# Performance work log

Measured on AMD Instinct MI355X. Metric: run time of the kernel, lower is better.

Reference implementation:

```python
import jax, jax.numpy as jnp
import numpy as np

N_EMBD = 1024
N_HEADS = 16
HEAD_DIM = N_EMBD // N_HEADS


def setup_inputs() -> dict:
    key = jax.random.key(0)
    ks = jax.random.split(key, 12)
    B, T, S, C = 2, 2048, 2048, N_EMBD
    std = 1.0 / np.sqrt(C)
    inp = {
        "x": jax.random.normal(ks[0], (B, T, C), dtype=jnp.float32),
        "context": jax.random.normal(ks[1], (B, S, C), dtype=jnp.float32),
        "q_w": jax.random.uniform(ks[2], (C, C), minval=-std, maxval=std, dtype=jnp.float32),
        "q_b": jax.random.uniform(ks[3], (C,), minval=-std, maxval=std, dtype=jnp.float32),
        "k_w": jax.random.uniform(ks[4], (C, C), minval=-std, maxval=std, dtype=jnp.float32),
        "k_b": jax.random.uniform(ks[5], (C,), minval=-std, maxval=std, dtype=jnp.float32),
        "v_w": jax.random.uniform(ks[6], (C, C), minval=-std, maxval=std, dtype=jnp.float32),
        "v_b": jax.random.uniform(ks[7], (C,), minval=-std, maxval=std, dtype=jnp.float32),
        "o_w": jax.random.uniform(ks[8], (C, C), minval=-std, maxval=std, dtype=jnp.float32),
        "o_b": jax.random.uniform(ks[9], (C,), minval=-std, maxval=std, dtype=jnp.float32),
    }
    return inp


def reference(x, context, q_w, q_b, k_w, k_b, v_w, v_b, o_w, o_b):
    B, T, C = x.shape
    S = context.shape[1]
    H, D = N_HEADS, HEAD_DIM
    # projections (torch Linear: y = x @ W^T + b; here weights stored as [in, out])
    q = (x @ q_w + q_b).reshape(B, T, H, D).transpose(0, 2, 1, 3)        # [B,H,T,D]
    k = (context @ k_w + k_b).reshape(B, S, H, D).transpose(0, 2, 1, 3)  # [B,H,S,D]
    v = (context @ v_w + v_b).reshape(B, S, H, D).transpose(0, 2, 1, 3)  # [B,H,S,D]
    att = jnp.einsum("bhtd,bhsd->bhts", q, k) / jnp.sqrt(jnp.float32(D))  # [B,H,T,S]
    causal = jnp.tril(jnp.ones((T, S), dtype=bool))                       # mask from tril buffer
    att = jnp.where(causal[None, None, :, :], att, -jnp.inf)
    att = jax.nn.softmax(att, axis=-1)
    y = jnp.einsum("bhts,bhsd->bhtd", att, v)                             # [B,H,T,D]
    y = y.transpose(0, 2, 1, 3).reshape(B, T, C)
    return y @ o_w + o_b
```

## Files before the change

### kernel.cpp

```cpp
#include <hip/hip_runtime.h>
#include <hip/hip_bf16.h>

using bf16 = __bf16;
using bf16x4 = __attribute__((ext_vector_type(4))) __bf16;
using bf16x8 = __attribute__((ext_vector_type(8))) __bf16;
using f32x4 = __attribute__((ext_vector_type(4))) float;

#define EXP2F(x) __builtin_amdgcn_exp2f(x)

__global__ __launch_bounds__(256) void cvt_kernel(const float4* __restrict__ a,
                                                  const float4* __restrict__ b,
                                                  bf16x4* __restrict__ out) {
  int g = blockIdx.x * blockDim.x + threadIdx.x;
  float4 v = (g < 1048576) ? a[g] : b[g - 1048576];
  bf16x4 o = {(bf16)v.x, (bf16)v.y, (bf16)v.z, (bf16)v.w};
  out[g] = o;
}

__global__ __launch_bounds__(256) void transpose_kernel(const float* __restrict__ w0,
                                                        const float* __restrict__ w1,
                                                        const float* __restrict__ w2,
                                                        const float* __restrict__ w3,
                                                        bf16* __restrict__ wtbase) {
  __shared__ float tile[32][33];
  const int z = blockIdx.z;
  const float* w = (z == 0) ? w0 : (z == 1) ? w1 : (z == 2) ? w2 : w3;
  bf16* wt = wtbase + (size_t)z * 1048576;
  int k0 = blockIdx.y * 32, n0 = blockIdx.x * 32;
  int tx = threadIdx.x, ty = threadIdx.y;
#pragma unroll
  for (int i = 0; i < 4; i++)
    tile[ty + i * 8][tx] = w[(size_t)(k0 + ty + i * 8) * 1024 + n0 + tx];
  __syncthreads();
#pragma unroll
  for (int i = 0; i < 4; i++)
    wt[(size_t)(n0 + ty + i * 8) * 1024 + k0 + tx] = (bf16)tile[tx][ty + i * 8];
}

__device__ __forceinline__ void gemm_body(const bf16* __restrict__ A,
                                          const bf16* __restrict__ Bt,
                                          const float* __restrict__ bias,
                                          void* __restrict__ outp, int mode, int bx, int by) {
  constexpr int K = 1024;
  __shared__ __align__(16) char smem[34816];
  bf16(*As)[40] = (bf16(*)[40])smem;
  bf16(*Bs)[40] = (bf16(*)[40])(smem + 10240);
  bf16(*Cs)[136] = (bf16(*)[136])smem;

  const int tid = threadIdx.x;
  const int lane = tid & 63;
  const int w = tid >> 6;
  const int wr = w >> 1, wc = w & 1;
  const int m0 = by * 128, n0 = bx * 128;
  const int fr = lane & 15, fg = (lane >> 4) * 8;

  f32x4 acc[4][4] = {};

  const int srow = tid >> 2;
  const int kc = (tid & 3) * 8;
  const int arow = m0 + srow, brow = n0 + srow;

  bf16x8 ra0, ra1, rb0, rb1;
  ra0 = *(const bf16x8*)&A[(size_t)arow * K + kc];
  ra1 = *(const bf16x8*)&A[(size_t)(arow + 64) * K + kc];
  rb0 = *(const bf16x8*)&Bt[(size_t)brow * K + kc];
  rb1 = *(const bf16x8*)&Bt[(size_t)(brow + 64) * K + kc];

  for (int k0 = 0; k0 < K; k0 += 32) {
    __syncthreads();
    *(bf16x8*)&As[srow][kc] = ra0;
    *(bf16x8*)&As[srow + 64][kc] = ra1;
    *(bf16x8*)&Bs[srow][kc] = rb0;
    *(bf16x8*)&Bs[srow + 64][kc] = rb1;
    if (k0 + 32 < K) {
      int kn = k0 + 32 + kc;
      ra0 = *(const bf16x8*)&A[(size_t)arow * K + kn];
      ra1 = *(const bf16x8*)&A[(size_t)(arow + 64) * K + kn];
      rb0 = *(const bf16x8*)&Bt[(size_t)brow * K + kn];
      rb1 = *(const bf16x8*)&Bt[(size_t)(brow + 64) * K + kn];
    }
    __syncthreads();
    bf16x8 af[4], bfr[4];
#pragma unroll
    for (int mi = 0; mi < 4; mi++)
      af[mi] = *(const bf16x8*)&As[wr * 64 + mi * 16 + fr][fg];
#pragma unroll
    for (int ni = 0; ni < 4; ni++)
      bfr[ni] = *(const bf16x8*)&Bs[wc * 64 + ni * 16 + fr][fg];
#pragma unroll
    for (int mi = 0; mi < 4; mi++)
#pragma unroll
      for (int ni = 0; ni < 4; ni++)
        acc[mi][ni] =
            __builtin_amdgcn_mfma_f32_16x16x32_bf16(af[mi], bfr[ni], acc[mi][ni], 0, 0, 0);
  }

  float bv[4];
#pragma unroll
  for (int ni = 0; ni < 4; ni++) bv[ni] = bias[n0 + wc * 64 + ni * 16 + fr];
#pragma unroll
  for (int mi = 0; mi < 4; mi++)
#pragma unroll
    for (int ni = 0; ni < 4; ni++)
#pragma unroll
      for (int j = 0; j < 4; j++) acc[mi][ni][j] += bv[ni];

  if (mode == 2) {
    float* O = (float*)outp;
#pragma unroll
    for (int mi = 0; mi < 4; mi++)
#pragma unroll
      for (int ni = 0; ni < 4; ni++)
#pragma unroll
        for (int j = 0; j < 4; j++) {
          int row = m0 + wr * 64 + mi * 16 + (lane >> 4) * 4 + j;
          int col = n0 + wc * 64 + ni * 16 + fr;
          O[(size_t)row * 1024 + col] = acc[mi][ni][j];
        }
    return;
  }

  __syncthreads();
#pragma unroll
  for (int mi = 0; mi < 4; mi++) {
    int r = wr * 64 + mi * 16 + (lane >> 4) * 4;
#pragma unroll
    for (int ni = 0; ni < 4; ni++) {
      int c = wc * 64 + ni * 16 + fr;
#pragma unroll
      for (int j = 0; j < 4; j++) Cs[r + j][c] = (bf16)acc[mi][ni][j];
    }
  }
  __syncthreads();

  bf16* O = (bf16*)outp;
  if (mode == 0) {
    int row = tid >> 1, ch = (tid & 1) * 64;
    int rg = m0 + row;
    int b = rg >> 11, t_ = rg & 2047;
    int c0 = n0 + ch;
    int h = c0 >> 6;
    bf16* dst = O + ((size_t)(b * 16 + h) * 2048 + t_) * 64;
#pragma unroll
    for (int i = 0; i < 8; i++) *(bf16x8*)&dst[i * 8] = *(const bf16x8*)&Cs[row][ch + i * 8];
  } else {
    int colL = tid >> 1, sh = (tid & 1) * 64;
    int cg = n0 + colL;
    int h = cg >> 6, d = cg & 63;
    int rg = m0 + sh;
    int b = rg >> 11, s_ = rg & 2047;
    bf16* dst = O + ((size_t)((b * 16 + h) * 64 + d)) * 2048 + s_;
#pragma unroll
    for (int i = 0; i < 8; i++) {
      bf16x8 v;
#pragma unroll
      for (int jj = 0; jj < 8; jj++) v[jj] = Cs[sh + i * 8 + jj][colL];
      *(bf16x8*)&dst[i * 8] = v;
    }
  }
}

__global__ __launch_bounds__(256) void gemm_qkv_kernel(const bf16* __restrict__ xb,
                                                       const bf16* __restrict__ cb,
                                                       const bf16* __restrict__ wtbase,
                                                       const float* __restrict__ bq,
                                                       const float* __restrict__ bk,
                                                       const float* __restrict__ bv,
                                                       bf16* __restrict__ outbase) {
  const int z = blockIdx.z;
  const bf16* A = (z == 0) ? xb : cb;
  const bf16* Wt = wtbase + (size_t)z * 1048576;
  const float* bias = (z == 0) ? bq : (z == 1) ? bk : bv;
  bf16* out = outbase + (size_t)z * 4194304;
  gemm_body(A, Wt, bias, (void*)out, (z == 2) ? 1 : 0, blockIdx.x, blockIdx.y);
}

__global__ __launch_bounds__(256) void gemm_o_kernel(const bf16* __restrict__ A,
                                                     const bf16* __restrict__ Wt,
                                                     const float* __restrict__ bias,
                                                     float* __restrict__ out) {
  gemm_body(A, Wt, bias, (void*)out, 2, blockIdx.x, blockIdx.y);
}

__global__ __launch_bounds__(256) void attn_kernel(const bf16* __restrict__ Q,
                                                   const bf16* __restrict__ Kc,
                                                   const bf16* __restrict__ Vt,
                                                   bf16* __restrict__ Y) {
  const int bh = blockIdx.x;
  const int qt = 31 - blockIdx.y;
  const int tid = threadIdx.x, lane = tid & 63, w = tid >> 6;
  const int lr = lane & 15, lg = lane >> 4;
  const int q0 = qt * 64 + w * 16;

  __shared__ __align__(16) bf16 Ks[64 * 64];
  __shared__ __align__(16) bf16 Vs[64 * 64];
  __shared__ __align__(16) bf16 Plds[4][16][72];

  const bf16* qb = Q + ((size_t)bh * 2048 + q0 + lr) * 64 + lg * 8;
  const bf16x8 qfB0 = *(const bf16x8*)qb;
  const bf16x8 qfB1 = *(const bf16x8*)(qb + 32);

  const bf16* Kbase = Kc + (size_t)bh * 2048 * 64;
  const bf16* Vbase = Vt + (size_t)bh * 64 * 2048;

  const int srow = tid >> 2;
  const int scol = (tid & 3) * 16;
  const int r7x = (srow & 7) * 8;
  const int d0 = srow * 64 + (scol ^ r7x);
  const int d1 = srow * 64 + ((scol + 8) ^ r7x);

  bf16x8 kr0, kr1, vr0, vr1;
  {
    const bf16* kp = Kbase + (size_t)srow * 64 + scol;
    kr0 = *(const bf16x8*)kp;
    kr1 = *(const bf16x8*)(kp + 8);
    const bf16* vp = Vbase + (size_t)srow * 2048 + scol;
    vr0 = *(const bf16x8*)vp;
    vr1 = *(const bf16x8*)(vp + 8);
  }

  f32x4 yacc[4] = {};
  float mrow = -__builtin_inff(), lrow = 0.0f;
  const float SCL = 0.125f * 1.4426950408889634f;
  const int kxor = (lr & 7) * 8;

  for (int c = 0; c <= qt; ++c) {
    const int sbase = c * 64;
    __syncthreads();
    *(bf16x8*)&Ks[d0] = kr0;
    *(bf16x8*)&Ks[d1] = kr1;
    *(bf16x8*)&Vs[d0] = vr0;
    *(bf16x8*)&Vs[d1] = vr1;
    __syncthreads();

    {
      const int cn = (c < qt) ? c + 1 : c;
      const int sb = cn * 64;
      const bf16* kp = Kbase + (size_t)(sb + srow) * 64 + scol;
      kr0 = *(const bf16x8*)kp;
      kr1 = *(const bf16x8*)(kp + 8);
      const bf16* vp = Vbase + (size_t)srow * 2048 + sb + scol;
      vr0 = *(const bf16x8*)vp;
      vr1 = *(const bf16x8*)(vp + 8);
    }

    f32x4 st[4];
#pragma unroll
    for (int h = 0; h < 4; ++h) {
      const int rb = (16 * h + lr) * 64;
      const bf16x8 kf0 = *(const bf16x8*)&Ks[rb + ((lg * 8) ^ kxor)];
      const bf16x8 kf1 = *(const bf16x8*)&Ks[rb + ((32 + lg * 8) ^ kxor)];
      f32x4 z = {};
      z = __builtin_amdgcn_mfma_f32_16x16x32_bf16(kf0, qfB0, z, 0, 0, 0);
      z = __builtin_amdgcn_mfma_f32_16x16x32_bf16(kf1, qfB1, z, 0, 0, 0);
      st[h] = z;
    }
#pragma unroll
    for (int h = 0; h < 4; ++h)
#pragma unroll
      for (int j = 0; j < 4; ++j) st[h][j] *= SCL;
    if (c == qt) {
      const int qg = q0 + lr;
#pragma unroll
      for (int h = 0; h < 4; ++h)
#pragma unroll
        for (int j = 0; j < 4; ++j) {
          int sg = sbase + 16 * h + lg * 4 + j;
          if (sg > qg) st[h][j] = -__builtin_inff();
        }
    }
    float vmax = fmaxf(fmaxf(st[0][0], st[0][1]), fmaxf(st[0][2], st[0][3]));
#pragma unroll
    for (int h = 1; h < 4; ++h)
      vmax = fmaxf(vmax, fmaxf(fmaxf(st[h][0], st[h][1]), fmaxf(st[h][2], st[h][3])));
    vmax = fmaxf(vmax, __shfl_xor(vmax, 16));
    vmax = fmaxf(vmax, __shfl_xor(vmax, 32));

    if (!__all(vmax <= mrow)) {
      const float mnew = fmaxf(mrow, vmax);
      const float cf = EXP2F(mrow - mnew);
      mrow = mnew;
      lrow *= cf;
      float cfj[4];
#pragma unroll
      for (int j = 0; j < 4; ++j) cfj[j] = __shfl(cf, lg * 4 + j);
#pragma unroll
      for (int nf = 0; nf < 4; ++nf)
#pragma unroll
        for (int j = 0; j < 4; ++j) yacc[nf][j] *= cfj[j];
    }

    float rs = 0.0f;
#pragma unroll
    for (int h = 0; h < 4; ++h) {
      float p0 = EXP2F(st[h][0] - mrow);
      float p1 = EXP2F(st[h][1] - mrow);
      float p2 = EXP2F(st[h][2] - mrow);
      float p3 = EXP2F(st[h][3] - mrow);
      rs += (p0 + p1) + (p2 + p3);
      bf16x4 pk = {(bf16)p0, (bf16)p1, (bf16)p2, (bf16)p3};
      *(bf16x4*)&Plds[w][lr][16 * h + lg * 4] = pk;
    }
    rs += __shfl_xor(rs, 16);
    rs += __shfl_xor(rs, 32);
    lrow += rs;

    const bf16x8 pa0 = *(const bf16x8*)&Plds[w][lr][lg * 8];
    const bf16x8 pa1 = *(const bf16x8*)&Plds[w][lr][32 + lg * 8];
#pragma unroll
    for (int nf = 0; nf < 4; ++nf) {
      const int rb = (nf * 16 + lr) * 64;
      const bf16x8 vf0 = *(const bf16x8*)&Vs[rb + ((lg * 8) ^ kxor)];
      const bf16x8 vf1 = *(const bf16x8*)&Vs[rb + ((32 + lg * 8) ^ kxor)];
      yacc[nf] = __builtin_amdgcn_mfma_f32_16x16x32_bf16(pa0, vf0, yacc[nf], 0, 0, 0);
      yacc[nf] = __builtin_amdgcn_mfma_f32_16x16x32_bf16(pa1, vf1, yacc[nf], 0, 0, 0);
    }
  }

  const float rinv = 1.0f / lrow;
  float linv[4];
#pragma unroll
  for (int j = 0; j < 4; ++j) linv[j] = __shfl(rinv, lg * 4 + j);
  const int b = bh >> 4, h = bh & 15;
#pragma unroll
  for (int nf = 0; nf < 4; ++nf)
#pragma unroll
    for (int j = 0; j < 4; ++j) {
      int qg = q0 + lg * 4 + j;
      Y[((size_t)b * 2048 + qg) * 1024 + h * 64 + nf * 16 + lr] = (bf16)(yacc[nf][j] * linv[j]);
    }
}

extern "C" void kernel_launch(void* const* d_in, const int* in_sizes, int n_in,
                              void* d_out, int out_size, void* d_ws, size_t ws_size,
                              hipStream_t stream) {
  const float* x = (const float*)d_in[0];
  const float* ctx = (const float*)d_in[1];
  const float* q_w = (const float*)d_in[2];
  const float* q_b = (const float*)d_in[3];
  const float* k_w = (const float*)d_in[4];
  const float* k_b = (const float*)d_in[5];
  const float* v_w = (const float*)d_in[6];
  const float* v_b = (const float*)d_in[7];
  const float* o_w = (const float*)d_in[8];
  const float* o_b = (const float*)d_in[9];

  char* ws = (char*)d_ws;
  const size_t MB = 1024 * 1024;
  bf16* xb = (bf16*)(ws + 0);
  bf16* qwt = (bf16*)(ws + 16 * MB);
  bf16* Qws = (bf16*)(ws + 24 * MB);
  bf16* Kws = (bf16*)(ws + 32 * MB);
  bf16* Vt = (bf16*)(ws + 40 * MB);
  bf16* Yws = (bf16*)(ws + 48 * MB);
  bf16* owt = qwt + 3 * 1048576;

  cvt_kernel<<<8192, 256, 0, stream>>>((const float4*)x, (const float4*)ctx, (bf16x4*)xb);

  dim3 tb(32, 8), tg(32, 32, 4);
  transpose_kernel<<<tg, tb, 0, stream>>>(q_w, k_w, v_w, o_w, qwt);

  bf16* cb = xb + (size_t)4096 * 1024 / 2 * 2;
  cb = xb + 4194304;
  gemm_qkv_kernel<<<dim3(8, 32, 3), 256, 0, stream>>>(xb, cb, qwt, q_b, k_b, v_b, Qws);

  attn_kernel<<<dim3(32, 32), 256, 0, stream>>>(Qws, Kws, Vt, Yws);

  gemm_o_kernel<<<dim3(8, 32), 256, 0, stream>>>(Yws, owt, o_b, (float*)d_out);
}
```

Baseline: 127.1 us.

## Remap GEMM blocks per XCD and split attention into 32-row query tiles

The QKV and output GEMMs now launch on a 1D grid and remap each block index so that consecutive tiles land on the same XCD, which should improve L2 locality on the multi-die GPU. The attention kernel moves from 64-row query tiles with 4 waves to 32-row tiles with 2 waves (128 threads). This doubles the block count and gives finer causal load balance. The trade-off is that each K/V chunk loaded into shared memory is now reused by half as many query rows, so total K/V load traffic goes up.

```diff
diff --git a/kernel.cpp b/kernel.cpp
--- a/kernel.cpp
+++ b/kernel.cpp
@@ -167,34 +167,44 @@
                                                        const float* __restrict__ bk,
                                                        const float* __restrict__ bv,
                                                        bf16* __restrict__ outbase) {
-  const int z = blockIdx.z;
+  const int lin = blockIdx.x;
+  const int xcd = lin & 7, idx = lin >> 3;
+  const int seq = xcd * 96 + idx;
+  const int z = seq >> 8;
+  const int rem = seq & 255;
+  const int by = rem >> 3, bx = rem & 7;
   const bf16* A = (z == 0) ? xb : cb;
   const bf16* Wt = wtbase + (size_t)z * 1048576;
   const float* bias = (z == 0) ? bq : (z == 1) ? bk : bv;
   bf16* out = outbase + (size_t)z * 4194304;
-  gemm_body(A, Wt, bias, (void*)out, (z == 2) ? 1 : 0, blockIdx.x, blockIdx.y);
+  gemm_body(A, Wt, bias, (void*)out, (z == 2) ? 1 : 0, bx, by);
 }
 
 __global__ __launch_bounds__(256) void gemm_o_kernel(const bf16* __restrict__ A,
                                                      const bf16* __restrict__ Wt,
                                                      const float* __restrict__ bias,
                                                      float* __restrict__ out) {
-  gemm_body(A, Wt, bias, (void*)out, 2, blockIdx.x, blockIdx.y);
-}
-
-__global__ __launch_bounds__(256) void attn_kernel(const bf16* __restrict__ Q,
+  const int lin = blockIdx.x;
+  const int xcd = lin & 7, idx = lin >> 3;
+  const int seq = xcd * 32 + idx;
+  const int by = seq >> 3, bx = seq & 7;
+  gemm_body(A, Wt, bias, (void*)out, 2, bx, by);
+}
+
+__global__ __launch_bounds__(128) void attn_kernel(const bf16* __restrict__ Q,
                                                    const bf16* __restrict__ Kc,
                                                    const bf16* __restrict__ Vt,
                                                    bf16* __restrict__ Y) {
   const int bh = blockIdx.x;
-  const int qt = 31 - blockIdx.y;
+  const int tile = 63 - blockIdx.y;
+  const int q0t = tile * 32;
   const int tid = threadIdx.x, lane = tid & 63, w = tid >> 6;
   const int lr = lane & 15, lg = lane >> 4;
-  const int q0 = qt * 64 + w * 16;
+  const int q0 = q0t + w * 16;
 
   __shared__ __align__(16) bf16 Ks[64 * 64];
   __shared__ __align__(16) bf16 Vs[64 * 64];
-  __shared__ __align__(16) bf16 Plds[4][16][72];
+  __shared__ __align__(16) bf16 Plds[2][16][72];
 
   const bf16* qb = Q + ((size_t)bh * 2048 + q0 + lr) * 64 + lg * 8;
   const bf16x8 qfB0 = *(const bf16x8*)qb;
@@ -203,45 +213,50 @@
   const bf16* Kbase = Kc + (size_t)bh * 2048 * 64;
   const bf16* Vbase = Vt + (size_t)bh * 64 * 2048;
 
-  const int srow = tid >> 2;
-  const int scol = (tid & 3) * 16;
+  const int srow = tid >> 1;
+  const int scol = (tid & 1) * 32;
   const int r7x = (srow & 7) * 8;
-  const int d0 = srow * 64 + (scol ^ r7x);
-  const int d1 = srow * 64 + ((scol + 8) ^ r7x);
-
-  bf16x8 kr0, kr1, vr0, vr1;
+  int dk[4];
+#pragma unroll
+  for (int i = 0; i < 4; ++i) dk[i] = srow * 64 + ((scol + i * 8) ^ r7x);
+
+  bf16x8 kr[4], vr[4];
   {
     const bf16* kp = Kbase + (size_t)srow * 64 + scol;
-    kr0 = *(const bf16x8*)kp;
-    kr1 = *(const bf16x8*)(kp + 8);
     const bf16* vp = Vbase + (size_t)srow * 2048 + scol;
-    vr0 = *(const bf16x8*)vp;
-    vr1 = *(const bf16x8*)(vp + 8);
+#pragma unroll
+    for (int i = 0; i < 4; ++i) {
+      kr[i] = *(const bf16x8*)(kp + i * 8);
+      vr[i] = *(const bf16x8*)(vp + i * 8);
+    }
   }
 
   f32x4 yacc[4] = {};
   float mrow = -__builtin_inff(), lrow = 0.0f;
   const float SCL = 0.125f * 1.4426950408889634f;
   const int kxor = (lr & 7) * 8;
-
-  for (int c = 0; c <= qt; ++c) {
+  const int nchunk = (q0t >> 6) + 1;
+
+  for (int c = 0; c < nchunk; ++c) {
     const int sbase = c * 64;
     __syncthreads();
-    *(bf16x8*)&Ks[d0] = kr0;
-    *(bf16x8*)&Ks[d1] = kr1;
-    *(bf16x8*)&Vs[d0] = vr0;
-    *(bf16x8*)&Vs[d1] = vr1;
+#pragma unroll
+    for (int i = 0; i < 4; ++i) {
+      *(bf16x8*)&Ks[dk[i]] = kr[i];
+      *(bf16x8*)&Vs[dk[i]] = vr[i];
+    }
     __syncthreads();
 
     {
-      const int cn = (c < qt) ? c + 1 : c;
+      const int cn = (c + 1 < nchunk) ? c + 1 : c;
       const int sb = cn * 64;
       const bf16* kp = Kbase + (size_t)(sb + srow) * 64 + scol;
-      kr0 = *(const bf16x8*)kp;
-      kr1 = *(const bf16x8*)(kp + 8);
       const bf16* vp = Vbase + (size_t)srow * 2048 + sb + scol;
-      vr0 = *(const bf16x8*)vp;
-      vr1 = *(const bf16x8*)(vp + 8);
+#pragma unroll
+      for (int i = 0; i < 4; ++i) {
+        kr[i] = *(const bf16x8*)(kp + i * 8);
+        vr[i] = *(const bf16x8*)(vp + i * 8);
+      }
     }
 
     f32x4 st[4];
@@ -259,7 +274,7 @@
     for (int h = 0; h < 4; ++h)
 #pragma unroll
       for (int j = 0; j < 4; ++j) st[h][j] *= SCL;
-    if (c == qt) {
+    if (c == nchunk - 1) {
       const int qg = q0 + lr;
 #pragma unroll
       for (int h = 0; h < 4; ++h)
@@ -354,17 +369,16 @@
   bf16* Vt = (bf16*)(ws + 40 * MB);
   bf16* Yws = (bf16*)(ws + 48 * MB);
   bf16* owt = qwt + 3 * 1048576;
+  bf16* cb = xb + 4194304;
 
   cvt_kernel<<<8192, 256, 0, stream>>>((const float4*)x, (const float4*)ctx, (bf16x4*)xb);
 
   dim3 tb(32, 8), tg(32, 32, 4);
   transpose_kernel<<<tg, tb, 0, stream>>>(q_w, k_w, v_w, o_w, qwt);
 
-  bf16* cb = xb + (size_t)4096 * 1024 / 2 * 2;
-  cb = xb + 4194304;
-  gemm_qkv_kernel<<<dim3(8, 32, 3), 256, 0, stream>>>(xb, cb, qwt, q_b, k_b, v_b, Qws);
-
-  attn_kernel<<<dim3(32, 32), 256, 0, stream>>>(Qws, Kws, Vt, Yws);
-
-  gemm_o_kernel<<<dim3(8, 32), 256, 0, stream>>>(Yws, owt, o_b, (float*)d_out);
-}
+  gemm_qkv_kernel<<<768, 256, 0, stream>>>(xb, cb, qwt, q_b, k_b, v_b, Qws);
+
+  attn_kernel<<<dim3(32, 64), 128, 0, stream>>>(Qws, Kws, Vt, Yws);
+
+  gemm_o_kernel<<<256, 256, 0, stream>>>(Yws, owt, o_b, (float*)d_out);
+}
```

Result: slower. 130.7 us (+2.8%).

## Fuse fp32-to-bf16 activation conversion into QKV GEMM, remap blocks per XCD

Applied to the files above, without the earlier changes.

Removes the separate cvt kernel: the QKV GEMM now loads fp32 activations directly and converts them to bf16 in registers. This avoids writing and re-reading a bf16 copy of x and context, though each GEMM tile now re-reads fp32 data at twice the byte width. The softmax scale is also folded into the Q projection epilogue, removing a multiply per score in the attention loop. Both GEMMs switch to a 1D grid whose block index is remapped so that consecutive tiles land on the same XCD, which is meant to improve L2 reuse.

```diff
diff --git a/kernel.cpp b/kernel.cpp
--- a/kernel.cpp
+++ b/kernel.cpp
@@ -7,15 +7,6 @@
 using f32x4 = __attribute__((ext_vector_type(4))) float;
 
 #define EXP2F(x) __builtin_amdgcn_exp2f(x)
-
-__global__ __launch_bounds__(256) void cvt_kernel(const float4* __restrict__ a,
-                                                  const float4* __restrict__ b,
-                                                  bf16x4* __restrict__ out) {
-  int g = blockIdx.x * blockDim.x + threadIdx.x;
-  float4 v = (g < 1048576) ? a[g] : b[g - 1048576];
-  bf16x4 o = {(bf16)v.x, (bf16)v.y, (bf16)v.z, (bf16)v.w};
-  out[g] = o;
-}
 
 __global__ __launch_bounds__(256) void transpose_kernel(const float* __restrict__ w0,
                                                         const float* __restrict__ w1,
@@ -37,10 +28,12 @@
     wt[(size_t)(n0 + ty + i * 8) * 1024 + k0 + tx] = (bf16)tile[tx][ty + i * 8];
 }
 
-__device__ __forceinline__ void gemm_body(const bf16* __restrict__ A,
+template <int MODE, bool AF32>
+__device__ __forceinline__ void gemm_body(const void* __restrict__ Ap,
                                           const bf16* __restrict__ Bt,
                                           const float* __restrict__ bias,
-                                          void* __restrict__ outp, int mode, int bx, int by) {
+                                          void* __restrict__ outp, int bx, int by,
+                                          float oscale) {
   constexpr int K = 1024;
   __shared__ __align__(16) char smem[34816];
   bf16(*As)[40] = (bf16(*)[40])smem;
@@ -60,9 +53,23 @@
   const int kc = (tid & 3) * 8;
   const int arow = m0 + srow, brow = n0 + srow;
 
+  auto loadA = [&](int row, int kcol) -> bf16x8 {
+    if constexpr (AF32) {
+      const float* Af = (const float*)Ap;
+      float4 u = *(const float4*)&Af[(size_t)row * K + kcol];
+      float4 v = *(const float4*)&Af[(size_t)row * K + kcol + 4];
+      bf16x8 r = {(bf16)u.x, (bf16)u.y, (bf16)u.z, (bf16)u.w,
+                  (bf16)v.x, (bf16)v.y, (bf16)v.z, (bf16)v.w};
+      return r;
+    } else {
+      const bf16* Ab = (const bf16*)Ap;
+      return *(const bf16x8*)&Ab[(size_t)row * K + kcol];
+    }
+  };
+
   bf16x8 ra0, ra1, rb0, rb1;
-  ra0 = *(const bf16x8*)&A[(size_t)arow * K + kc];
-  ra1 = *(const bf16x8*)&A[(size_t)(arow + 64) * K + kc];
+  ra0 = loadA(arow, kc);
+  ra1 = loadA(arow + 64, kc);
   rb0 = *(const bf16x8*)&Bt[(size_t)brow * K + kc];
   rb1 = *(const bf16x8*)&Bt[(size_t)(brow + 64) * K + kc];
 
@@ -74,8 +81,8 @@
     *(bf16x8*)&Bs[srow + 64][kc] = rb1;
     if (k0 + 32 < K) {
       int kn = k0 + 32 + kc;
-      ra0 = *(const bf16x8*)&A[(size_t)arow * K + kn];
-      ra1 = *(const bf16x8*)&A[(size_t)(arow + 64) * K + kn];
+      ra0 = loadA(arow, kn);
+      ra1 = loadA(arow + 64, kn);
       rb0 = *(const bf16x8*)&Bt[(size_t)brow * K + kn];
       rb1 = *(const bf16x8*)&Bt[(size_t)(brow + 64) * K + kn];
     }
@@ -103,9 +110,9 @@
 #pragma unroll
     for (int ni = 0; ni < 4; ni++)
 #pragma unroll
-      for (int j = 0; j < 4; j++) acc[mi][ni][j] += bv[ni];
-
-  if (mode == 2) {
+      for (int j = 0; j < 4; j++) acc[mi][ni][j] = (acc[mi][ni][j] + bv[ni]) * oscale;
+
+  if (MODE == 2) {
     float* O = (float*)outp;
 #pragma unroll
     for (int mi = 0; mi < 4; mi++)
@@ -134,7 +141,7 @@
   __syncthreads();
 
   bf16* O = (bf16*)outp;
-  if (mode == 0) {
+  if (MODE == 0) {
     int row = tid >> 1, ch = (tid & 1) * 64;
     int rg = m0 + row;
     int b = rg >> 11, t_ = rg & 2047;
@@ -160,26 +167,39 @@
   }
 }
 
-__global__ __launch_bounds__(256) void gemm_qkv_kernel(const bf16* __restrict__ xb,
-                                                       const bf16* __restrict__ cb,
+__global__ __launch_bounds__(256) void gemm_qkv_kernel(const float* __restrict__ x,
+                                                       const float* __restrict__ ctx,
                                                        const bf16* __restrict__ wtbase,
                                                        const float* __restrict__ bq,
                                                        const float* __restrict__ bk,
                                                        const float* __restrict__ bv,
                                                        bf16* __restrict__ outbase) {
-  const int z = blockIdx.z;
-  const bf16* A = (z == 0) ? xb : cb;
+  const int lin = blockIdx.x;
+  const int xcd = lin & 7, idx = lin >> 3;
+  const int seq = xcd * 96 + idx;
+  const int z = seq >> 8;
+  const int rem = seq & 255;
+  const int by = rem >> 3, bx = rem & 7;
+  const float* A = (z == 0) ? x : ctx;
   const bf16* Wt = wtbase + (size_t)z * 1048576;
   const float* bias = (z == 0) ? bq : (z == 1) ? bk : bv;
   bf16* out = outbase + (size_t)z * 4194304;
-  gemm_body(A, Wt, bias, (void*)out, (z == 2) ? 1 : 0, blockIdx.x, blockIdx.y);
+  const float oscale = (z == 0) ? 0.125f * 1.4426950408889634f : 1.0f;
+  if (z == 2)
+    gemm_body<1, true>(A, Wt, bias, (void*)out, bx, by, oscale);
+  else
+    gemm_body<0, true>(A, Wt, bias, (void*)out, bx, by, oscale);
 }
 
 __global__ __launch_bounds__(256) void gemm_o_kernel(const bf16* __restrict__ A,
                                                      const bf16* __restrict__ Wt,
                                                      const float* __restrict__ bias,
                                                      float* __restrict__ out) {
-  gemm_body(A, Wt, bias, (void*)out, 2, blockIdx.x, blockIdx.y);
+  const int lin = blockIdx.x;
+  const int xcd = lin & 7, idx = lin >> 3;
+  const int seq = xcd * 32 + idx;
+  const int by = seq >> 3, bx = seq & 7;
+  gemm_body<2, false>(A, Wt, bias, (void*)out, bx, by, 1.0f);
 }
 
 __global__ __launch_bounds__(256) void attn_kernel(const bf16* __restrict__ Q,
@@ -221,7 +241,6 @@
 
   f32x4 yacc[4] = {};
   float mrow = -__builtin_inff(), lrow = 0.0f;
-  const float SCL = 0.125f * 1.4426950408889634f;
   const int kxor = (lr & 7) * 8;
 
   for (int c = 0; c <= qt; ++c) {
@@ -255,10 +274,6 @@
       z = __builtin_amdgcn_mfma_f32_16x16x32_bf16(kf1, qfB1, z, 0, 0, 0);
       st[h] = z;
     }
-#pragma unroll
-    for (int h = 0; h < 4; ++h)
-#pragma unroll
-      for (int j = 0; j < 4; ++j) st[h][j] *= SCL;
     if (c == qt) {
       const int qg = q0 + lr;
 #pragma unroll
@@ -347,24 +362,19 @@
 
   char* ws = (char*)d_ws;
   const size_t MB = 1024 * 1024;
-  bf16* xb = (bf16*)(ws + 0);
-  bf16* qwt = (bf16*)(ws + 16 * MB);
-  bf16* Qws = (bf16*)(ws + 24 * MB);
-  bf16* Kws = (bf16*)(ws + 32 * MB);
-  bf16* Vt = (bf16*)(ws + 40 * MB);
-  bf16* Yws = (bf16*)(ws + 48 * MB);
+  bf16* qwt = (bf16*)(ws + 0);
+  bf16* Qws = (bf16*)(ws + 8 * MB);
+  bf16* Kws = (bf16*)(ws + 16 * MB);
+  bf16* Vt = (bf16*)(ws + 24 * MB);
+  bf16* Yws = (bf16*)(ws + 32 * MB);
   bf16* owt = qwt + 3 * 1048576;
-
-  cvt_kernel<<<8192, 256, 0, stream>>>((const float4*)x, (const float4*)ctx, (bf16x4*)xb);
 
   dim3 tb(32, 8), tg(32, 32, 4);
   transpose_kernel<<<tg, tb, 0, stream>>>(q_w, k_w, v_w, o_w, qwt);
 
-  bf16* cb = xb + (size_t)4096 * 1024 / 2 * 2;
-  cb = xb + 4194304;
-  gemm_qkv_kernel<<<dim3(8, 32, 3), 256, 0, stream>>>(xb, cb, qwt, q_b, k_b, v_b, Qws);
+  gemm_qkv_kernel<<<768, 256, 0, stream>>>(x, ctx, qwt, q_b, k_b, v_b, Qws);
 
   attn_kernel<<<dim3(32, 32), 256, 0, stream>>>(Qws, Kws, Vt, Yws);
 
-  gemm_o_kernel<<<dim3(8, 32), 256, 0, stream>>>(Yws, owt, o_b, (float*)d_out);
-}
+  gemm_o_kernel<<<256, 256, 0, stream>>>(Yws, owt, o_b, (float*)d_out);
+}
```

Measured after the change: 129.7 us. 2.0% more time.
